# Kernel optimization log

Hardware: AMD Instinct MI355X
Metric: run time of the kernel (lower is better)

The kernel has to match this reference:

```python
import jax, jax.numpy as jnp
import numpy as np

SLACKNESS_PENALTY = 1.0
WEIGHT_DECAY = 1e-5

POS_LEN, NUM_NEG = 32768, 64
N_RULES, N_UNLABEL = 262144, 131072
NUM_ENT, NUM_REL, EMB_DIM = 100000, 500, 256


def _rand_triples(key, n):
    k1, k2, k3 = jax.random.split(key, 3)
    h = jax.random.randint(k1, (n,), 0, NUM_ENT)
    r = jax.random.randint(k2, (n,), 0, NUM_REL)
    t = jax.random.randint(k3, (n,), 0, NUM_ENT)
    return jnp.stack([h, r, t], axis=1)  # [n, 3]


def setup_inputs() -> dict:
    key = jax.random.key(0)
    ks = jax.random.split(key, 10)
    pos_score = jax.random.normal(ks[0], (POS_LEN, 1), dtype=jnp.float32)
    neg_score = jax.random.normal(ks[1], (POS_LEN, NUM_NEG), dtype=jnp.float32)
    confidence = jax.random.uniform(ks[2], (N_RULES,), dtype=jnp.float32)
    ent_emb = jax.random.normal(ks[3], (NUM_ENT, EMB_DIM), dtype=jnp.float32) * 0.1
    rel_emb = jax.random.normal(ks[4], (NUM_REL, EMB_DIM), dtype=jnp.float32) * 0.1
    rule_p1 = _rand_triples(ks[5], N_RULES)
    rule_p2 = _rand_triples(ks[6], N_RULES)
    triple_num = jax.random.randint(ks[7], (N_RULES,), 2, 4)  # values in {2, 3}
    unlabel_ids = jax.random.randint(ks[8], (N_RULES,), 0, N_UNLABEL)
    unlabel_triples = _rand_triples(ks[9], N_UNLABEL)
    return dict(pos_score=pos_score, neg_score=neg_score, confidence=confidence,
                ent_emb=ent_emb, rel_emb=rel_emb, rule_p1=rule_p1, rule_p2=rule_p2,
                triple_num=triple_num, unlabel_ids=unlabel_ids,
                unlabel_triples=unlabel_triples)


def _score(triples, ent_emb, rel_emb):
    # DistMult KGE score: sum_d e_h * w_r * e_t  -> [n, 1]
    h = ent_emb[triples[:, 0]]
    r = rel_emb[triples[:, 1]]
    t = ent_emb[triples[:, 2]]
    return jnp.sum(h * r * t, axis=-1, keepdims=True)


def reference(pos_score, neg_score, confidence, ent_emb, rel_emb,
              rule_p1, rule_p2, triple_num, unlabel_ids, unlabel_triples):
    # BCE(sigmoid(pos), 1) = softplus(-x); BCE(sigmoid(neg), 0) = softplus(x)
    positive_loss = jnp.mean(jax.nn.softplus(-pos_score))
    negative_loss = jnp.mean(jax.nn.softplus(neg_score))

    # Per-rule body sigmoids (originally memoized one-row model() calls)
    s1 = jax.nn.sigmoid(_score(rule_p1, ent_emb, rel_emb))[:, 0]  # [n_rules]
    s2 = jax.nn.sigmoid(_score(rule_p2, ent_emb, rel_emb))[:, 0]
    contrib = SLACKNESS_PENALTY * confidence * s1 * jnp.where(triple_num == 3, s2, 1.0)
    # pi_gradient dict scatter-add -> segment_sum over unique unlabel triples
    pi_grad = jax.ops.segment_sum(contrib, unlabel_ids,
                                  num_segments=unlabel_triples.shape[0])  # [n_unlabel]

    su = _score(unlabel_triples, ent_emb, rel_emb)  # [n_unlabel, 1]
    p = jax.nn.sigmoid(su)
    # target = clip(p + pi_grad, 0, 1), detached (original uses .cpu().detach().numpy())
    tgt = jax.lax.stop_gradient(jnp.clip(p + pi_grad[:, None], 0.0, 1.0))
    # BCE(p, tgt) with stable log-sigmoid forms
    unlabel_loss = jnp.mean(tgt * jax.nn.softplus(-su) + (1.0 - tgt) * jax.nn.softplus(su))

    regularization = WEIGHT_DECAY * (jnp.sum(ent_emb ** 2) + jnp.sum(rel_emb ** 2))
    return positive_loss + negative_loss + unlabel_loss + regularization
```

## Files before the change

kernel.cpp:

```cpp
#include <hip/hip_runtime.h>
#include <cstddef>
#include <cstdint>

#define POS_LEN    32768
#define NUM_NEG    64
#define N_RULES    262144
#define N_UNLABEL  131072
#define NUM_ENT    100000
#define NUM_REL    500
#define EMB_DIM    256
#define WEIGHT_DECAY 1e-5

#define AUX_BLOCKS    2048
#define GATHER_BLOCKS 2048
#define LOSS_BLOCKS   256

typedef __attribute__((ext_vector_type(4))) float        f32x4;
typedef __attribute__((ext_vector_type(2))) unsigned int u32x2;

__device__ __forceinline__ float softplusf_(float x) {
    return fmaxf(x, 0.0f) + log1pf(expf(-fabsf(x)));
}
__device__ __forceinline__ float sigmoidf_(float x) {
    return 1.0f / (1.0f + expf(-x));
}
__device__ __forceinline__ float half_sum32(float v) {
#pragma unroll
    for (int m = 1; m <= 16; m <<= 1) v += __shfl_xor(v, m, 64);
    return v;
}
__device__ __forceinline__ float wave_sum64(float v) {
#pragma unroll
    for (int m = 32; m >= 1; m >>= 1) v += __shfl_xor(v, m, 64);
    return v;
}
__device__ __forceinline__ double wave_sum64d(double v) {
#pragma unroll
    for (int m = 32; m >= 1; m >>= 1) v += __shfl_xor(v, m, 64);
    return v;
}

__device__ __forceinline__ u32x2 f32x8_to_fp8(const f32x4 a, const f32x4 b) {
    int lo = 0, hi = 0;
    lo = __builtin_amdgcn_cvt_pk_fp8_f32(a[0], a[1], lo, false);
    lo = __builtin_amdgcn_cvt_pk_fp8_f32(a[2], a[3], lo, true);
    hi = __builtin_amdgcn_cvt_pk_fp8_f32(b[0], b[1], hi, false);
    hi = __builtin_amdgcn_cvt_pk_fp8_f32(b[2], b[3], hi, true);
    u32x2 r; r[0] = (unsigned)lo; r[1] = (unsigned)hi; return r;
}
__device__ __forceinline__ void fp8x4_to_f32(unsigned int w, float* o) {
    auto x = __builtin_amdgcn_cvt_pk_f32_fp8((int)w, false);
    auto y = __builtin_amdgcn_cvt_pk_f32_fp8((int)w, true);
    o[0] = x[0]; o[1] = x[1]; o[2] = y[0]; o[3] = y[1];
}

__device__ __forceinline__ float triple_score_fp8(const u32x2* __restrict__ ent8,
                                                  const u32x2* __restrict__ rel8,
                                                  int h, int r, int t, int l) {
    const u32x2 hv = ent8[(size_t)h * 32 + l];
    const u32x2 rv = rel8[(size_t)r * 32 + l];
    const u32x2 tv = ent8[(size_t)t * 32 + l];
    float hf[8], rf[8], tf[8];
    fp8x4_to_f32(hv[0], hf); fp8x4_to_f32(hv[1], hf + 4);
    fp8x4_to_f32(rv[0], rf); fp8x4_to_f32(rv[1], rf + 4);
    fp8x4_to_f32(tv[0], tf); fp8x4_to_f32(tv[1], tf + 4);
    float s = 0.0f;
#pragma unroll
    for (int j = 0; j < 8; ++j) s = fmaf(hf[j] * rf[j], tf[j], s);
    return half_sum32(s);
}

__global__ void aux_convert_kernel(const float* __restrict__ pos,
                                   const float* __restrict__ neg,
                                   const float* __restrict__ ent,
                                   const float* __restrict__ rel,
                                   u32x2* __restrict__ ent8,
                                   u32x2* __restrict__ rel8,
                                   float* __restrict__ pi_grad,
                                   float* __restrict__ auxp) {
    const int tid = blockIdx.x * blockDim.x + threadIdx.x;
    const int stride = gridDim.x * blockDim.x;

    for (int i = tid; i < N_UNLABEL; i += stride) pi_grad[i] = 0.0f;

    float ps = 0.0f, ns = 0.0f, sq = 0.0f;
    const f32x4* posv = reinterpret_cast<const f32x4*>(pos);
    const f32x4* negv = reinterpret_cast<const f32x4*>(neg);
    for (int i = tid; i < POS_LEN / 4; i += stride) {
        f32x4 v = __builtin_nontemporal_load(posv + i);
        ps += softplusf_(-v[0]) + softplusf_(-v[1]) + softplusf_(-v[2]) + softplusf_(-v[3]);
    }
    for (int i = tid; i < (POS_LEN * NUM_NEG) / 4; i += stride) {
        f32x4 v = __builtin_nontemporal_load(negv + i);
        ns += softplusf_(v[0]) + softplusf_(v[1]) + softplusf_(v[2]) + softplusf_(v[3]);
    }
    const f32x4* entv = reinterpret_cast<const f32x4*>(ent);
    for (int i = tid; i < (NUM_ENT * EMB_DIM) / 8; i += stride) {
        f32x4 a = __builtin_nontemporal_load(entv + (size_t)i * 2);
        f32x4 b = __builtin_nontemporal_load(entv + (size_t)i * 2 + 1);
        sq += a[0]*a[0] + a[1]*a[1] + a[2]*a[2] + a[3]*a[3]
            + b[0]*b[0] + b[1]*b[1] + b[2]*b[2] + b[3]*b[3];
        ent8[i] = f32x8_to_fp8(a, b);
    }
    const f32x4* relv = reinterpret_cast<const f32x4*>(rel);
    for (int i = tid; i < (NUM_REL * EMB_DIM) / 8; i += stride) {
        f32x4 a = __builtin_nontemporal_load(relv + (size_t)i * 2);
        f32x4 b = __builtin_nontemporal_load(relv + (size_t)i * 2 + 1);
        sq += a[0]*a[0] + a[1]*a[1] + a[2]*a[2] + a[3]*a[3]
            + b[0]*b[0] + b[1]*b[1] + b[2]*b[2] + b[3]*b[3];
        rel8[i] = f32x8_to_fp8(a, b);
    }

    ps = wave_sum64(ps); ns = wave_sum64(ns); sq = wave_sum64(sq);
    __shared__ float lp[8], ln[8], ls[8];
    const int lane = threadIdx.x & 63, wid = threadIdx.x >> 6;
    if (lane == 0) { lp[wid] = ps; ln[wid] = ns; ls[wid] = sq; }
    __syncthreads();
    if (threadIdx.x == 0) {
        float bp = 0.0f, bn = 0.0f, bs = 0.0f;
        for (int w = 0; w < (int)(blockDim.x >> 6); ++w) { bp += lp[w]; bn += ln[w]; bs += ls[w]; }
        auxp[blockIdx.x]                  = bp;
        auxp[AUX_BLOCKS + blockIdx.x]     = bn;
        auxp[2 * AUX_BLOCKS + blockIdx.x] = bs;
    }
}

__global__ void gather_kernel(const float* __restrict__ conf,
                              const u32x2* __restrict__ ent8,
                              const u32x2* __restrict__ rel8,
                              const int* __restrict__ p1,
                              const int* __restrict__ p2,
                              const int* __restrict__ tnum,
                              const int* __restrict__ uids,
                              const int* __restrict__ ut,
                              float* __restrict__ pi_grad,
                              float* __restrict__ su_out) {
    const int lane = threadIdx.x & 63;
    const int l    = lane & 31;
    const int half = lane >> 5;
    const int wave  = blockIdx.x * (blockDim.x >> 6) + (threadIdx.x >> 6);
    const int nwave = gridDim.x * (blockDim.x >> 6);
    const int nrp = N_RULES / 2, nup = N_UNLABEL / 2, ntot = nrp + nup;

    for (int pi = wave; pi < ntot; pi += nwave) {
        if (pi < nrp) {
            const int rule = pi * 2 + half;
            const int h1 = p1[rule * 3 + 0], r1 = p1[rule * 3 + 1], t1 = p1[rule * 3 + 2];
            float c = sigmoidf_(triple_score_fp8(ent8, rel8, h1, r1, t1, l)) * conf[rule];
            if (tnum[rule] == 3) {
                const int h2 = p2[rule * 3 + 0], r2 = p2[rule * 3 + 1], t2 = p2[rule * 3 + 2];
                c *= sigmoidf_(triple_score_fp8(ent8, rel8, h2, r2, t2, l));
            }
            if (l == 0) atomicAdd(&pi_grad[uids[rule]], c);
        } else {
            const int i = (pi - nrp) * 2 + half;
            const int h = ut[i * 3 + 0], r = ut[i * 3 + 1], t = ut[i * 3 + 2];
            const float su = triple_score_fp8(ent8, rel8, h, r, t, l);
            if (l == 0) su_out[i] = su;
        }
    }
}

__global__ void loss_kernel(const float* __restrict__ su,
                            const float* __restrict__ pi_grad,
                            float* __restrict__ lossp) {
    const int tid = blockIdx.x * blockDim.x + threadIdx.x;
    const int stride = gridDim.x * blockDim.x;
    float acc = 0.0f;
    for (int i = tid; i < N_UNLABEL; i += stride) {
        const float s   = su[i];
        const float p   = sigmoidf_(s);
        const float tgt = fminf(fmaxf(p + pi_grad[i], 0.0f), 1.0f);
        acc += tgt * softplusf_(-s) + (1.0f - tgt) * softplusf_(s);
    }
    acc = wave_sum64(acc);
    __shared__ float part[8];
    const int lane = threadIdx.x & 63, wid = threadIdx.x >> 6;
    if (lane == 0) part[wid] = acc;
    __syncthreads();
    if (threadIdx.x == 0) {
        float b = 0.0f;
        for (int w = 0; w < (int)(blockDim.x >> 6); ++w) b += part[w];
        lossp[blockIdx.x] = b;
    }
}

__global__ void finalize_kernel(const float* __restrict__ auxp,
                                const float* __restrict__ lossp,
                                float* __restrict__ out) {
    const int lane = threadIdx.x;
    double ps = 0.0, ns = 0.0, sq = 0.0, ul = 0.0;
    for (int i = lane; i < AUX_BLOCKS; i += 64) {
        ps += (double)auxp[i];
        ns += (double)auxp[AUX_BLOCKS + i];
        sq += (double)auxp[2 * AUX_BLOCKS + i];
    }
    for (int i = lane; i < LOSS_BLOCKS; i += 64) ul += (double)lossp[i];
    ps = wave_sum64d(ps); ns = wave_sum64d(ns);
    sq = wave_sum64d(sq); ul = wave_sum64d(ul);
    if (lane == 0) {
        double v = ps / (double)POS_LEN
                 + ns / ((double)POS_LEN * (double)NUM_NEG)
                 + ul / (double)N_UNLABEL
                 + WEIGHT_DECAY * sq;
        out[0] = (float)v;
    }
}

extern "C" void kernel_launch(void* const* d_in, const int* in_sizes, int n_in,
                              void* d_out, int out_size, void* d_ws, size_t ws_size,
                              hipStream_t stream) {
    const float* pos  = (const float*)d_in[0];
    const float* neg  = (const float*)d_in[1];
    const float* conf = (const float*)d_in[2];
    const float* ent  = (const float*)d_in[3];
    const float* rel  = (const float*)d_in[4];
    const int*   p1   = (const int*)d_in[5];
    const int*   p2   = (const int*)d_in[6];
    const int*   tnum = (const int*)d_in[7];
    const int*   uids = (const int*)d_in[8];
    const int*   ut   = (const int*)d_in[9];

    const size_t off_pi    = 0;
    const size_t off_su    = off_pi + (size_t)N_UNLABEL * 4;
    const size_t off_auxp  = off_su + (size_t)N_UNLABEL * 4;
    const size_t off_lossp = off_auxp + (size_t)3 * AUX_BLOCKS * 4;
    const size_t off_ent8  = (off_lossp + (size_t)LOSS_BLOCKS * 4 + 511) & ~(size_t)511;
    const size_t off_rel8  = off_ent8 + (size_t)NUM_ENT * EMB_DIM;

    float* pi_grad = (float*)((char*)d_ws + off_pi);
    float* su      = (float*)((char*)d_ws + off_su);
    float* auxp    = (float*)((char*)d_ws + off_auxp);
    float* lossp   = (float*)((char*)d_ws + off_lossp);
    u32x2* ent8    = (u32x2*)((char*)d_ws + off_ent8);
    u32x2* rel8    = (u32x2*)((char*)d_ws + off_rel8);

    aux_convert_kernel<<<AUX_BLOCKS, 256, 0, stream>>>(pos, neg, ent, rel,
                                                       ent8, rel8, pi_grad, auxp);
    gather_kernel<<<GATHER_BLOCKS, 256, 0, stream>>>(conf, ent8, rel8, p1, p2, tnum,
                                                     uids, ut, pi_grad, su);
    loss_kernel<<<LOSS_BLOCKS, 256, 0, stream>>>(su, pi_grad, lossp);
    finalize_kernel<<<1, 64, 0, stream>>>(auxp, lossp, (float*)d_out);
}
```

Before: 108.8 us.

## Use fp16 embedding tables with fdot2 and move pos/neg loss into loss kernel

Adds an fp16 path, chosen when the workspace is large enough, that converts the embedding tables to half precision. The gather computes scores with packed fdot2, using 16 lanes per triple and four triples per wave. The pos/neg softplus reductions move from the conversion kernel into the loss kernel, which gets more blocks. The fp16 tables double table write and gather bytes compared with fp8, in exchange for fewer lanes per triple, higher accuracy, and cheaper dot products.

New measurement: 132.7 us. 1.22x slower.

```diff
diff --git a/kernel.cpp b/kernel.cpp
--- a/kernel.cpp
+++ b/kernel.cpp
@@ -13,10 +13,11 @@
 
 #define AUX_BLOCKS    2048
 #define GATHER_BLOCKS 2048
-#define LOSS_BLOCKS   256
+#define LOSS_BLOCKS   1024
 
 typedef __attribute__((ext_vector_type(4))) float        f32x4;
 typedef __attribute__((ext_vector_type(2))) unsigned int u32x2;
+typedef __attribute__((ext_vector_type(8))) _Float16     h8;
 
 __device__ __forceinline__ float softplusf_(float x) {
     return fmaxf(x, 0.0f) + log1pf(expf(-fabsf(x)));
@@ -24,6 +25,11 @@
 __device__ __forceinline__ float sigmoidf_(float x) {
     return 1.0f / (1.0f + expf(-x));
 }
+__device__ __forceinline__ float quarter_sum16(float v) {
+#pragma unroll
+    for (int m = 1; m <= 8; m <<= 1) v += __shfl_xor(v, m, 64);
+    return v;
+}
 __device__ __forceinline__ float half_sum32(float v) {
 #pragma unroll
     for (int m = 1; m <= 16; m <<= 1) v += __shfl_xor(v, m, 64);
@@ -38,6 +44,43 @@
 #pragma unroll
     for (int m = 32; m >= 1; m >>= 1) v += __shfl_xor(v, m, 64);
     return v;
+}
+
+__device__ __forceinline__ h8 f32x8_to_h8(const f32x4 a, const f32x4 b) {
+    auto p0 = __builtin_amdgcn_cvt_pkrtz(a[0], a[1]);
+    auto p1 = __builtin_amdgcn_cvt_pkrtz(a[2], a[3]);
+    auto p2 = __builtin_amdgcn_cvt_pkrtz(b[0], b[1]);
+    auto p3 = __builtin_amdgcn_cvt_pkrtz(b[2], b[3]);
+    h8 o;
+    o[0] = (_Float16)p0[0]; o[1] = (_Float16)p0[1];
+    o[2] = (_Float16)p1[0]; o[3] = (_Float16)p1[1];
+    o[4] = (_Float16)p2[0]; o[5] = (_Float16)p2[1];
+    o[6] = (_Float16)p3[0]; o[7] = (_Float16)p3[1];
+    return o;
+}
+
+#define FD2(acc, m, t, i0, i1)                                               \
+    acc = __builtin_amdgcn_fdot2(                                            \
+        __builtin_shufflevector(m, m, i0, i1),                               \
+        __builtin_shufflevector(t, t, i0, i1), acc, false)
+
+__device__ __forceinline__ float triple_score_f16(const h8* __restrict__ ent16,
+                                                  const h8* __restrict__ rel16,
+                                                  int h, int r, int t, int l) {
+    const h8* hp = ent16 + (size_t)h * 32 + l * 2;
+    const h8* rp = rel16 + (size_t)r * 32 + l * 2;
+    const h8* tp = ent16 + (size_t)t * 32 + l * 2;
+    h8 h0 = hp[0], h1 = hp[1];
+    h8 r0 = rp[0], r1 = rp[1];
+    h8 t0 = tp[0], t1 = tp[1];
+    h8 m0 = h0 * r0;
+    h8 m1 = h1 * r1;
+    float acc = 0.0f;
+    FD2(acc, m0, t0, 0, 1); FD2(acc, m0, t0, 2, 3);
+    FD2(acc, m0, t0, 4, 5); FD2(acc, m0, t0, 6, 7);
+    FD2(acc, m1, t1, 0, 1); FD2(acc, m1, t1, 2, 3);
+    FD2(acc, m1, t1, 4, 5); FD2(acc, m1, t1, 6, 7);
+    return quarter_sum16(acc);
 }
 
 __device__ __forceinline__ u32x2 f32x8_to_fp8(const f32x4 a, const f32x4 b) {
@@ -53,7 +96,6 @@
     auto y = __builtin_amdgcn_cvt_pk_f32_fp8((int)w, true);
     o[0] = x[0]; o[1] = x[1]; o[2] = y[0]; o[3] = y[1];
 }
-
 __device__ __forceinline__ float triple_score_fp8(const u32x2* __restrict__ ent8,
                                                   const u32x2* __restrict__ rel8,
                                                   int h, int r, int t, int l) {
@@ -70,30 +112,55 @@
     return half_sum32(s);
 }
 
-__global__ void aux_convert_kernel(const float* __restrict__ pos,
-                                   const float* __restrict__ neg,
-                                   const float* __restrict__ ent,
-                                   const float* __restrict__ rel,
-                                   u32x2* __restrict__ ent8,
-                                   u32x2* __restrict__ rel8,
-                                   float* __restrict__ pi_grad,
-                                   float* __restrict__ auxp) {
+__global__ void aux_f16_kernel(const float* __restrict__ ent,
+                               const float* __restrict__ rel,
+                               h8* __restrict__ ent16,
+                               h8* __restrict__ rel16,
+                               float* __restrict__ pi_grad,
+                               float* __restrict__ auxp) {
     const int tid = blockIdx.x * blockDim.x + threadIdx.x;
     const int stride = gridDim.x * blockDim.x;
-
     for (int i = tid; i < N_UNLABEL; i += stride) pi_grad[i] = 0.0f;
 
-    float ps = 0.0f, ns = 0.0f, sq = 0.0f;
-    const f32x4* posv = reinterpret_cast<const f32x4*>(pos);
-    const f32x4* negv = reinterpret_cast<const f32x4*>(neg);
-    for (int i = tid; i < POS_LEN / 4; i += stride) {
-        f32x4 v = __builtin_nontemporal_load(posv + i);
-        ps += softplusf_(-v[0]) + softplusf_(-v[1]) + softplusf_(-v[2]) + softplusf_(-v[3]);
-    }
-    for (int i = tid; i < (POS_LEN * NUM_NEG) / 4; i += stride) {
-        f32x4 v = __builtin_nontemporal_load(negv + i);
-        ns += softplusf_(v[0]) + softplusf_(v[1]) + softplusf_(v[2]) + softplusf_(v[3]);
-    }
+    float sq = 0.0f;
+    const f32x4* entv = reinterpret_cast<const f32x4*>(ent);
+    for (int i = tid; i < (NUM_ENT * EMB_DIM) / 8; i += stride) {
+        f32x4 a = __builtin_nontemporal_load(entv + (size_t)i * 2);
+        f32x4 b = __builtin_nontemporal_load(entv + (size_t)i * 2 + 1);
+        sq += a[0]*a[0] + a[1]*a[1] + a[2]*a[2] + a[3]*a[3]
+            + b[0]*b[0] + b[1]*b[1] + b[2]*b[2] + b[3]*b[3];
+        ent16[i] = f32x8_to_h8(a, b);
+    }
+    const f32x4* relv = reinterpret_cast<const f32x4*>(rel);
+    for (int i = tid; i < (NUM_REL * EMB_DIM) / 8; i += stride) {
+        f32x4 a = __builtin_nontemporal_load(relv + (size_t)i * 2);
+        f32x4 b = __builtin_nontemporal_load(relv + (size_t)i * 2 + 1);
+        sq += a[0]*a[0] + a[1]*a[1] + a[2]*a[2] + a[3]*a[3]
+            + b[0]*b[0] + b[1]*b[1] + b[2]*b[2] + b[3]*b[3];
+        rel16[i] = f32x8_to_h8(a, b);
+    }
+    sq = wave_sum64(sq);
+    __shared__ float ls[8];
+    const int lane = threadIdx.x & 63, wid = threadIdx.x >> 6;
+    if (lane == 0) ls[wid] = sq;
+    __syncthreads();
+    if (threadIdx.x == 0) {
+        float bs = 0.0f;
+        for (int w = 0; w < (int)(blockDim.x >> 6); ++w) bs += ls[w];
+        auxp[blockIdx.x] = bs;
+    }
+}
+
+__global__ void aux_fp8_kernel(const float* __restrict__ ent,
+                               const float* __restrict__ rel,
+                               u32x2* __restrict__ ent8,
+                               u32x2* __restrict__ rel8,
+                               float* __restrict__ pi_grad,
+                               float* __restrict__ auxp) {
+    const int tid = blockIdx.x * blockDim.x + threadIdx.x;
+    const int stride = gridDim.x * blockDim.x;
+    for (int i = tid; i < N_UNLABEL; i += stride) pi_grad[i] = 0.0f;
+    float sq = 0.0f;
     const f32x4* entv = reinterpret_cast<const f32x4*>(ent);
     for (int i = tid; i < (NUM_ENT * EMB_DIM) / 8; i += stride) {
         f32x4 a = __builtin_nontemporal_load(entv + (size_t)i * 2);
@@ -110,38 +177,70 @@
             + b[0]*b[0] + b[1]*b[1] + b[2]*b[2] + b[3]*b[3];
         rel8[i] = f32x8_to_fp8(a, b);
     }
-
-    ps = wave_sum64(ps); ns = wave_sum64(ns); sq = wave_sum64(sq);
-    __shared__ float lp[8], ln[8], ls[8];
+    sq = wave_sum64(sq);
+    __shared__ float ls[8];
     const int lane = threadIdx.x & 63, wid = threadIdx.x >> 6;
-    if (lane == 0) { lp[wid] = ps; ln[wid] = ns; ls[wid] = sq; }
+    if (lane == 0) ls[wid] = sq;
     __syncthreads();
     if (threadIdx.x == 0) {
-        float bp = 0.0f, bn = 0.0f, bs = 0.0f;
-        for (int w = 0; w < (int)(blockDim.x >> 6); ++w) { bp += lp[w]; bn += ln[w]; bs += ls[w]; }
-        auxp[blockIdx.x]                  = bp;
-        auxp[AUX_BLOCKS + blockIdx.x]     = bn;
-        auxp[2 * AUX_BLOCKS + blockIdx.x] = bs;
-    }
-}
-
-__global__ void gather_kernel(const float* __restrict__ conf,
-                              const u32x2* __restrict__ ent8,
-                              const u32x2* __restrict__ rel8,
-                              const int* __restrict__ p1,
-                              const int* __restrict__ p2,
-                              const int* __restrict__ tnum,
-                              const int* __restrict__ uids,
-                              const int* __restrict__ ut,
-                              float* __restrict__ pi_grad,
-                              float* __restrict__ su_out) {
+        float bs = 0.0f;
+        for (int w = 0; w < (int)(blockDim.x >> 6); ++w) bs += ls[w];
+        auxp[blockIdx.x] = bs;
+    }
+}
+
+__global__ void gather_f16_kernel(const float* __restrict__ conf,
+                                  const h8* __restrict__ ent16,
+                                  const h8* __restrict__ rel16,
+                                  const int* __restrict__ p1,
+                                  const int* __restrict__ p2,
+                                  const int* __restrict__ tnum,
+                                  const int* __restrict__ uids,
+                                  const int* __restrict__ ut,
+                                  float* __restrict__ pi_grad,
+                                  float* __restrict__ su_out) {
+    const int lane = threadIdx.x & 63;
+    const int l    = lane & 15;
+    const int q    = lane >> 4;
+    const int wave  = blockIdx.x * (blockDim.x >> 6) + (threadIdx.x >> 6);
+    const int nwave = gridDim.x * (blockDim.x >> 6);
+    const int nr4 = N_RULES / 4, nu4 = N_UNLABEL / 4, ntot = nr4 + nu4;
+
+    for (int pi = wave; pi < ntot; pi += nwave) {
+        if (pi < nr4) {
+            const int rule = pi * 4 + q;
+            const int h1 = p1[rule * 3 + 0], r1 = p1[rule * 3 + 1], t1 = p1[rule * 3 + 2];
+            float c = sigmoidf_(triple_score_f16(ent16, rel16, h1, r1, t1, l)) * conf[rule];
+            if (tnum[rule] == 3) {
+                const int h2 = p2[rule * 3 + 0], r2 = p2[rule * 3 + 1], t2 = p2[rule * 3 + 2];
+                c *= sigmoidf_(triple_score_f16(ent16, rel16, h2, r2, t2, l));
+            }
+            if (l == 0) atomicAdd(&pi_grad[uids[rule]], c);
+        } else {
+            const int i = (pi - nr4) * 4 + q;
+            const int h = ut[i * 3 + 0], r = ut[i * 3 + 1], t = ut[i * 3 + 2];
+            const float su = triple_score_f16(ent16, rel16, h, r, t, l);
+            if (l == 0) su_out[i] = su;
+        }
+    }
+}
+
+__global__ void gather_fp8_kernel(const float* __restrict__ conf,
+                                  const u32x2* __restrict__ ent8,
+                                  const u32x2* __restrict__ rel8,
+                                  const int* __restrict__ p1,
+                                  const int* __restrict__ p2,
+                                  const int* __restrict__ tnum,
+                                  const int* __restrict__ uids,
+                                  const int* __restrict__ ut,
+                                  float* __restrict__ pi_grad,
+                                  float* __restrict__ su_out) {
     const int lane = threadIdx.x & 63;
     const int l    = lane & 31;
     const int half = lane >> 5;
     const int wave  = blockIdx.x * (blockDim.x >> 6) + (threadIdx.x >> 6);
     const int nwave = gridDim.x * (blockDim.x >> 6);
     const int nrp = N_RULES / 2, nup = N_UNLABEL / 2, ntot = nrp + nup;
-
     for (int pi = wave; pi < ntot; pi += nwave) {
         if (pi < nrp) {
             const int rule = pi * 2 + half;
@@ -163,25 +262,39 @@
 
 __global__ void loss_kernel(const float* __restrict__ su,
                             const float* __restrict__ pi_grad,
+                            const float* __restrict__ pos,
+                            const float* __restrict__ neg,
                             float* __restrict__ lossp) {
     const int tid = blockIdx.x * blockDim.x + threadIdx.x;
     const int stride = gridDim.x * blockDim.x;
-    float acc = 0.0f;
+    float ul = 0.0f, ps = 0.0f, ns = 0.0f;
     for (int i = tid; i < N_UNLABEL; i += stride) {
         const float s   = su[i];
         const float p   = sigmoidf_(s);
         const float tgt = fminf(fmaxf(p + pi_grad[i], 0.0f), 1.0f);
-        acc += tgt * softplusf_(-s) + (1.0f - tgt) * softplusf_(s);
-    }
-    acc = wave_sum64(acc);
-    __shared__ float part[8];
+        ul += tgt * softplusf_(-s) + (1.0f - tgt) * softplusf_(s);
+    }
+    const f32x4* posv = reinterpret_cast<const f32x4*>(pos);
+    for (int i = tid; i < POS_LEN / 4; i += stride) {
+        f32x4 v = __builtin_nontemporal_load(posv + i);
+        ps += softplusf_(-v[0]) + softplusf_(-v[1]) + softplusf_(-v[2]) + softplusf_(-v[3]);
+    }
+    const f32x4* negv = reinterpret_cast<const f32x4*>(neg);
+    for (int i = tid; i < (POS_LEN * NUM_NEG) / 4; i += stride) {
+        f32x4 v = __builtin_nontemporal_load(negv + i);
+        ns += softplusf_(v[0]) + softplusf_(v[1]) + softplusf_(v[2]) + softplusf_(v[3]);
+    }
+    ul = wave_sum64(ul); ps = wave_sum64(ps); ns = wave_sum64(ns);
+    __shared__ float lu[8], lp[8], ln[8];
     const int lane = threadIdx.x & 63, wid = threadIdx.x >> 6;
-    if (lane == 0) part[wid] = acc;
+    if (lane == 0) { lu[wid] = ul; lp[wid] = ps; ln[wid] = ns; }
     __syncthreads();
     if (threadIdx.x == 0) {
-        float b = 0.0f;
-        for (int w = 0; w < (int)(blockDim.x >> 6); ++w) b += part[w];
-        lossp[blockIdx.x] = b;
+        float bu = 0.0f, bp = 0.0f, bn = 0.0f;
+        for (int w = 0; w < (int)(blockDim.x >> 6); ++w) { bu += lu[w]; bp += lp[w]; bn += ln[w]; }
+        lossp[blockIdx.x]                   = bu;
+        lossp[LOSS_BLOCKS + blockIdx.x]     = bp;
+        lossp[2 * LOSS_BLOCKS + blockIdx.x] = bn;
     }
 }
 
@@ -189,15 +302,15 @@
                                 const float* __restrict__ lossp,
                                 float* __restrict__ out) {
     const int lane = threadIdx.x;
-    double ps = 0.0, ns = 0.0, sq = 0.0, ul = 0.0;
-    for (int i = lane; i < AUX_BLOCKS; i += 64) {
-        ps += (double)auxp[i];
-        ns += (double)auxp[AUX_BLOCKS + i];
-        sq += (double)auxp[2 * AUX_BLOCKS + i];
-    }
-    for (int i = lane; i < LOSS_BLOCKS; i += 64) ul += (double)lossp[i];
+    double sq = 0.0, ul = 0.0, ps = 0.0, ns = 0.0;
+    for (int i = lane; i < AUX_BLOCKS; i += 64) sq += (double)auxp[i];
+    for (int i = lane; i < LOSS_BLOCKS; i += 64) {
+        ul += (double)lossp[i];
+        ps += (double)lossp[LOSS_BLOCKS + i];
+        ns += (double)lossp[2 * LOSS_BLOCKS + i];
+    }
+    sq = wave_sum64d(sq); ul = wave_sum64d(ul);
     ps = wave_sum64d(ps); ns = wave_sum64d(ns);
-    sq = wave_sum64d(sq); ul = wave_sum64d(ul);
     if (lane == 0) {
         double v = ps / (double)POS_LEN
                  + ns / ((double)POS_LEN * (double)NUM_NEG)
@@ -224,21 +337,28 @@
     const size_t off_pi    = 0;
     const size_t off_su    = off_pi + (size_t)N_UNLABEL * 4;
     const size_t off_auxp  = off_su + (size_t)N_UNLABEL * 4;
-    const size_t off_lossp = off_auxp + (size_t)3 * AUX_BLOCKS * 4;
-    const size_t off_ent8  = (off_lossp + (size_t)LOSS_BLOCKS * 4 + 511) & ~(size_t)511;
-    const size_t off_rel8  = off_ent8 + (size_t)NUM_ENT * EMB_DIM;
+    const size_t off_lossp = off_auxp + (size_t)AUX_BLOCKS * 4;
+    const size_t off_tab   = (off_lossp + (size_t)3 * LOSS_BLOCKS * 4 + 511) & ~(size_t)511;
+    const size_t f16_need  = off_tab + (size_t)(NUM_ENT + NUM_REL) * EMB_DIM * 2;
 
     float* pi_grad = (float*)((char*)d_ws + off_pi);
     float* su      = (float*)((char*)d_ws + off_su);
     float* auxp    = (float*)((char*)d_ws + off_auxp);
     float* lossp   = (float*)((char*)d_ws + off_lossp);
-    u32x2* ent8    = (u32x2*)((char*)d_ws + off_ent8);
-    u32x2* rel8    = (u32x2*)((char*)d_ws + off_rel8);
-
-    aux_convert_kernel<<<AUX_BLOCKS, 256, 0, stream>>>(pos, neg, ent, rel,
-                                                       ent8, rel8, pi_grad, auxp);
-    gather_kernel<<<GATHER_BLOCKS, 256, 0, stream>>>(conf, ent8, rel8, p1, p2, tnum,
-                                                     uids, ut, pi_grad, su);
-    loss_kernel<<<LOSS_BLOCKS, 256, 0, stream>>>(su, pi_grad, lossp);
+
+    if (ws_size >= f16_need) {
+        h8* ent16 = (h8*)((char*)d_ws + off_tab);
+        h8* rel16 = (h8*)((char*)d_ws + off_tab + (size_t)NUM_ENT * EMB_DIM * 2);
+        aux_f16_kernel<<<AUX_BLOCKS, 256, 0, stream>>>(ent, rel, ent16, rel16, pi_grad, auxp);
+        gather_f16_kernel<<<GATHER_BLOCKS, 256, 0, stream>>>(conf, ent16, rel16, p1, p2,
+                                                             tnum, uids, ut, pi_grad, su);
+    } else {
+        u32x2* ent8 = (u32x2*)((char*)d_ws + off_tab);
+        u32x2* rel8 = (u32x2*)((char*)d_ws + off_tab + (size_t)NUM_ENT * EMB_DIM);
+        aux_fp8_kernel<<<AUX_BLOCKS, 256, 0, stream>>>(ent, rel, ent8, rel8, pi_grad, auxp);
+        gather_fp8_kernel<<<GATHER_BLOCKS, 256, 0, stream>>>(conf, ent8, rel8, p1, p2,
+                                                             tnum, uids, ut, pi_grad, su);
+    }
+    loss_kernel<<<LOSS_BLOCKS, 256, 0, stream>>>(su, pi_grad, pos, neg, lossp);
     finalize_kernel<<<1, 64, 0, stream>>>(auxp, lossp, (float*)d_out);
 }
```

## Gather fp8 rows with 16-byte loads and move pos/neg softplus into loss kernel

Applied to the files above, without the earlier changes.

The gather kernel now assigns 16 lanes per triple, so each lane loads 16 bytes of fp8 embedding and a wave scores four triples at once. It also issues the second body's loads before computing the first score, to expose more memory parallelism. The pos/neg softplus reductions move from the convert kernel into the loss kernel, whose grid grows from 256 to 1024 blocks. This shortens the critical path before the gather, but puts the 8 MB negative-score read after the gather on the same stream.

Measured after the change: 101.3 us. 6.8% less time.

```diff
diff --git a/kernel.cpp b/kernel.cpp
--- a/kernel.cpp
+++ b/kernel.cpp
@@ -13,10 +13,11 @@
 
 #define AUX_BLOCKS    2048
 #define GATHER_BLOCKS 2048
-#define LOSS_BLOCKS   256
+#define LOSS_BLOCKS   1024
 
 typedef __attribute__((ext_vector_type(4))) float        f32x4;
 typedef __attribute__((ext_vector_type(2))) unsigned int u32x2;
+typedef __attribute__((ext_vector_type(4))) unsigned int u32x4;
 
 __device__ __forceinline__ float softplusf_(float x) {
     return fmaxf(x, 0.0f) + log1pf(expf(-fabsf(x)));
@@ -24,9 +25,9 @@
 __device__ __forceinline__ float sigmoidf_(float x) {
     return 1.0f / (1.0f + expf(-x));
 }
-__device__ __forceinline__ float half_sum32(float v) {
-#pragma unroll
-    for (int m = 1; m <= 16; m <<= 1) v += __shfl_xor(v, m, 64);
+__device__ __forceinline__ float quarter_sum16(float v) {
+#pragma unroll
+    for (int m = 1; m <= 8; m <<= 1) v += __shfl_xor(v, m, 64);
     return v;
 }
 __device__ __forceinline__ float wave_sum64(float v) {
@@ -54,46 +55,32 @@
     o[0] = x[0]; o[1] = x[1]; o[2] = y[0]; o[3] = y[1];
 }
 
-__device__ __forceinline__ float triple_score_fp8(const u32x2* __restrict__ ent8,
-                                                  const u32x2* __restrict__ rel8,
-                                                  int h, int r, int t, int l) {
-    const u32x2 hv = ent8[(size_t)h * 32 + l];
-    const u32x2 rv = rel8[(size_t)r * 32 + l];
-    const u32x2 tv = ent8[(size_t)t * 32 + l];
-    float hf[8], rf[8], tf[8];
-    fp8x4_to_f32(hv[0], hf); fp8x4_to_f32(hv[1], hf + 4);
-    fp8x4_to_f32(rv[0], rf); fp8x4_to_f32(rv[1], rf + 4);
-    fp8x4_to_f32(tv[0], tf); fp8x4_to_f32(tv[1], tf + 4);
+__device__ __forceinline__ float dot3_q(const u32x4 hv, const u32x4 rv, const u32x4 tv) {
     float s = 0.0f;
 #pragma unroll
-    for (int j = 0; j < 8; ++j) s = fmaf(hf[j] * rf[j], tf[j], s);
-    return half_sum32(s);
-}
-
-__global__ void aux_convert_kernel(const float* __restrict__ pos,
-                                   const float* __restrict__ neg,
-                                   const float* __restrict__ ent,
-                                   const float* __restrict__ rel,
-                                   u32x2* __restrict__ ent8,
-                                   u32x2* __restrict__ rel8,
-                                   float* __restrict__ pi_grad,
-                                   float* __restrict__ auxp) {
+    for (int w = 0; w < 4; ++w) {
+        float hf[4], rf[4], tf[4];
+        fp8x4_to_f32(hv[w], hf);
+        fp8x4_to_f32(rv[w], rf);
+        fp8x4_to_f32(tv[w], tf);
+        s = fmaf(hf[0] * rf[0], tf[0], s);
+        s = fmaf(hf[1] * rf[1], tf[1], s);
+        s = fmaf(hf[2] * rf[2], tf[2], s);
+        s = fmaf(hf[3] * rf[3], tf[3], s);
+    }
+    return quarter_sum16(s);
+}
+
+__global__ void aux_fp8_kernel(const float* __restrict__ ent,
+                               const float* __restrict__ rel,
+                               u32x2* __restrict__ ent8,
+                               u32x2* __restrict__ rel8,
+                               float* __restrict__ pi_grad,
+                               float* __restrict__ auxp) {
     const int tid = blockIdx.x * blockDim.x + threadIdx.x;
     const int stride = gridDim.x * blockDim.x;
-
     for (int i = tid; i < N_UNLABEL; i += stride) pi_grad[i] = 0.0f;
-
-    float ps = 0.0f, ns = 0.0f, sq = 0.0f;
-    const f32x4* posv = reinterpret_cast<const f32x4*>(pos);
-    const f32x4* negv = reinterpret_cast<const f32x4*>(neg);
-    for (int i = tid; i < POS_LEN / 4; i += stride) {
-        f32x4 v = __builtin_nontemporal_load(posv + i);
-        ps += softplusf_(-v[0]) + softplusf_(-v[1]) + softplusf_(-v[2]) + softplusf_(-v[3]);
-    }
-    for (int i = tid; i < (POS_LEN * NUM_NEG) / 4; i += stride) {
-        f32x4 v = __builtin_nontemporal_load(negv + i);
-        ns += softplusf_(v[0]) + softplusf_(v[1]) + softplusf_(v[2]) + softplusf_(v[3]);
-    }
+    float sq = 0.0f;
     const f32x4* entv = reinterpret_cast<const f32x4*>(ent);
     for (int i = tid; i < (NUM_ENT * EMB_DIM) / 8; i += stride) {
         f32x4 a = __builtin_nontemporal_load(entv + (size_t)i * 2);
@@ -110,24 +97,21 @@
             + b[0]*b[0] + b[1]*b[1] + b[2]*b[2] + b[3]*b[3];
         rel8[i] = f32x8_to_fp8(a, b);
     }
-
-    ps = wave_sum64(ps); ns = wave_sum64(ns); sq = wave_sum64(sq);
-    __shared__ float lp[8], ln[8], ls[8];
+    sq = wave_sum64(sq);
+    __shared__ float ls[8];
     const int lane = threadIdx.x & 63, wid = threadIdx.x >> 6;
-    if (lane == 0) { lp[wid] = ps; ln[wid] = ns; ls[wid] = sq; }
+    if (lane == 0) ls[wid] = sq;
     __syncthreads();
     if (threadIdx.x == 0) {
-        float bp = 0.0f, bn = 0.0f, bs = 0.0f;
-        for (int w = 0; w < (int)(blockDim.x >> 6); ++w) { bp += lp[w]; bn += ln[w]; bs += ls[w]; }
-        auxp[blockIdx.x]                  = bp;
-        auxp[AUX_BLOCKS + blockIdx.x]     = bn;
-        auxp[2 * AUX_BLOCKS + blockIdx.x] = bs;
+        float bs = 0.0f;
+        for (int w = 0; w < (int)(blockDim.x >> 6); ++w) bs += ls[w];
+        auxp[blockIdx.x] = bs;
     }
 }
 
 __global__ void gather_kernel(const float* __restrict__ conf,
-                              const u32x2* __restrict__ ent8,
-                              const u32x2* __restrict__ rel8,
+                              const u32x4* __restrict__ ent8,
+                              const u32x4* __restrict__ rel8,
                               const int* __restrict__ p1,
                               const int* __restrict__ p2,
                               const int* __restrict__ tnum,
@@ -136,26 +120,42 @@
                               float* __restrict__ pi_grad,
                               float* __restrict__ su_out) {
     const int lane = threadIdx.x & 63;
-    const int l    = lane & 31;
-    const int half = lane >> 5;
+    const int l    = lane & 15;
+    const int q    = lane >> 4;
     const int wave  = blockIdx.x * (blockDim.x >> 6) + (threadIdx.x >> 6);
     const int nwave = gridDim.x * (blockDim.x >> 6);
-    const int nrp = N_RULES / 2, nup = N_UNLABEL / 2, ntot = nrp + nup;
+    const int nr4 = N_RULES / 4, nu4 = N_UNLABEL / 4, ntot = nr4 + nu4;
 
     for (int pi = wave; pi < ntot; pi += nwave) {
-        if (pi < nrp) {
-            const int rule = pi * 2 + half;
-            const int h1 = p1[rule * 3 + 0], r1 = p1[rule * 3 + 1], t1 = p1[rule * 3 + 2];
-            float c = sigmoidf_(triple_score_fp8(ent8, rel8, h1, r1, t1, l)) * conf[rule];
-            if (tnum[rule] == 3) {
-                const int h2 = p2[rule * 3 + 0], r2 = p2[rule * 3 + 1], t2 = p2[rule * 3 + 2];
-                c *= sigmoidf_(triple_score_fp8(ent8, rel8, h2, r2, t2, l));
+        if (pi < nr4) {
+            const int rule = pi * 4 + q;
+            const int b = rule * 3;
+            const int h1 = p1[b], r1 = p1[b + 1], t1 = p1[b + 2];
+            const int tn = tnum[rule];
+            const float cf = conf[rule];
+            const int uid = uids[rule];
+            const bool has2 = (tn == 3);
+            const u32x4 H1 = ent8[(size_t)h1 * 16 + l];
+            const u32x4 R1 = rel8[(size_t)r1 * 16 + l];
+            const u32x4 T1 = ent8[(size_t)t1 * 16 + l];
+            u32x4 H2 = {0, 0, 0, 0}, R2 = {0, 0, 0, 0}, T2 = {0, 0, 0, 0};
+            if (has2) {
+                const int h2 = p2[b], r2 = p2[b + 1], t2 = p2[b + 2];
+                H2 = ent8[(size_t)h2 * 16 + l];
+                R2 = rel8[(size_t)r2 * 16 + l];
+                T2 = ent8[(size_t)t2 * 16 + l];
             }
-            if (l == 0) atomicAdd(&pi_grad[uids[rule]], c);
+            float c = sigmoidf_(dot3_q(H1, R1, T1)) * cf;
+            if (has2) c *= sigmoidf_(dot3_q(H2, R2, T2));
+            if (l == 0) atomicAdd(&pi_grad[uid], c);
         } else {
-            const int i = (pi - nrp) * 2 + half;
-            const int h = ut[i * 3 + 0], r = ut[i * 3 + 1], t = ut[i * 3 + 2];
-            const float su = triple_score_fp8(ent8, rel8, h, r, t, l);
+            const int i = (pi - nr4) * 4 + q;
+            const int b = i * 3;
+            const int h = ut[b], r = ut[b + 1], t = ut[b + 2];
+            const u32x4 H = ent8[(size_t)h * 16 + l];
+            const u32x4 R = rel8[(size_t)r * 16 + l];
+            const u32x4 T = ent8[(size_t)t * 16 + l];
+            const float su = dot3_q(H, R, T);
             if (l == 0) su_out[i] = su;
         }
     }
@@ -163,25 +163,39 @@
 
 __global__ void loss_kernel(const float* __restrict__ su,
                             const float* __restrict__ pi_grad,
+                            const float* __restrict__ pos,
+                            const float* __restrict__ neg,
                             float* __restrict__ lossp) {
     const int tid = blockIdx.x * blockDim.x + threadIdx.x;
     const int stride = gridDim.x * blockDim.x;
-    float acc = 0.0f;
+    float ul = 0.0f, ps = 0.0f, ns = 0.0f;
     for (int i = tid; i < N_UNLABEL; i += stride) {
         const float s   = su[i];
         const float p   = sigmoidf_(s);
         const float tgt = fminf(fmaxf(p + pi_grad[i], 0.0f), 1.0f);
-        acc += tgt * softplusf_(-s) + (1.0f - tgt) * softplusf_(s);
-    }
-    acc = wave_sum64(acc);
-    __shared__ float part[8];
+        ul += tgt * softplusf_(-s) + (1.0f - tgt) * softplusf_(s);
+    }
+    const f32x4* posv = reinterpret_cast<const f32x4*>(pos);
+    for (int i = tid; i < POS_LEN / 4; i += stride) {
+        f32x4 v = __builtin_nontemporal_load(posv + i);
+        ps += softplusf_(-v[0]) + softplusf_(-v[1]) + softplusf_(-v[2]) + softplusf_(-v[3]);
+    }
+    const f32x4* negv = reinterpret_cast<const f32x4*>(neg);
+    for (int i = tid; i < (POS_LEN * NUM_NEG) / 4; i += stride) {
+        f32x4 v = __builtin_nontemporal_load(negv + i);
+        ns += softplusf_(v[0]) + softplusf_(v[1]) + softplusf_(v[2]) + softplusf_(v[3]);
+    }
+    ul = wave_sum64(ul); ps = wave_sum64(ps); ns = wave_sum64(ns);
+    __shared__ float lu[8], lp[8], ln[8];
     const int lane = threadIdx.x & 63, wid = threadIdx.x >> 6;
-    if (lane == 0) part[wid] = acc;
+    if (lane == 0) { lu[wid] = ul; lp[wid] = ps; ln[wid] = ns; }
     __syncthreads();
     if (threadIdx.x == 0) {
-        float b = 0.0f;
-        for (int w = 0; w < (int)(blockDim.x >> 6); ++w) b += part[w];
-        lossp[blockIdx.x] = b;
+        float bu = 0.0f, bp = 0.0f, bn = 0.0f;
+        for (int w = 0; w < (int)(blockDim.x >> 6); ++w) { bu += lu[w]; bp += lp[w]; bn += ln[w]; }
+        lossp[blockIdx.x]                   = bu;
+        lossp[LOSS_BLOCKS + blockIdx.x]     = bp;
+        lossp[2 * LOSS_BLOCKS + blockIdx.x] = bn;
     }
 }
 
@@ -189,15 +203,15 @@
                                 const float* __restrict__ lossp,
                                 float* __restrict__ out) {
     const int lane = threadIdx.x;
-    double ps = 0.0, ns = 0.0, sq = 0.0, ul = 0.0;
-    for (int i = lane; i < AUX_BLOCKS; i += 64) {
-        ps += (double)auxp[i];
-        ns += (double)auxp[AUX_BLOCKS + i];
-        sq += (double)auxp[2 * AUX_BLOCKS + i];
-    }
-    for (int i = lane; i < LOSS_BLOCKS; i += 64) ul += (double)lossp[i];
+    double sq = 0.0, ul = 0.0, ps = 0.0, ns = 0.0;
+    for (int i = lane; i < AUX_BLOCKS; i += 64) sq += (double)auxp[i];
+    for (int i = lane; i < LOSS_BLOCKS; i += 64) {
+        ul += (double)lossp[i];
+        ps += (double)lossp[LOSS_BLOCKS + i];
+        ns += (double)lossp[2 * LOSS_BLOCKS + i];
+    }
+    sq = wave_sum64d(sq); ul = wave_sum64d(ul);
     ps = wave_sum64d(ps); ns = wave_sum64d(ns);
-    sq = wave_sum64d(sq); ul = wave_sum64d(ul);
     if (lane == 0) {
         double v = ps / (double)POS_LEN
                  + ns / ((double)POS_LEN * (double)NUM_NEG)
@@ -224,21 +238,22 @@
     const size_t off_pi    = 0;
     const size_t off_su    = off_pi + (size_t)N_UNLABEL * 4;
     const size_t off_auxp  = off_su + (size_t)N_UNLABEL * 4;
-    const size_t off_lossp = off_auxp + (size_t)3 * AUX_BLOCKS * 4;
-    const size_t off_ent8  = (off_lossp + (size_t)LOSS_BLOCKS * 4 + 511) & ~(size_t)511;
-    const size_t off_rel8  = off_ent8 + (size_t)NUM_ENT * EMB_DIM;
+    const size_t off_lossp = off_auxp + (size_t)AUX_BLOCKS * 4;
+    const size_t off_tab   = (off_lossp + (size_t)3 * LOSS_BLOCKS * 4 + 511) & ~(size_t)511;
+    const size_t off_rel8  = off_tab + (size_t)NUM_ENT * EMB_DIM;
 
     float* pi_grad = (float*)((char*)d_ws + off_pi);
     float* su      = (float*)((char*)d_ws + off_su);
     float* auxp    = (float*)((char*)d_ws + off_auxp);
     float* lossp   = (float*)((char*)d_ws + off_lossp);
-    u32x2* ent8    = (u32x2*)((char*)d_ws + off_ent8);
-    u32x2* rel8    = (u32x2*)((char*)d_ws + off_rel8);
-
-    aux_convert_kernel<<<AUX_BLOCKS, 256, 0, stream>>>(pos, neg, ent, rel,
-                                                       ent8, rel8, pi_grad, auxp);
-    gather_kernel<<<GATHER_BLOCKS, 256, 0, stream>>>(conf, ent8, rel8, p1, p2, tnum,
-                                                     uids, ut, pi_grad, su);
-    loss_kernel<<<LOSS_BLOCKS, 256, 0, stream>>>(su, pi_grad, lossp);
+    u32x2* ent8w   = (u32x2*)((char*)d_ws + off_tab);
+    u32x2* rel8w   = (u32x2*)((char*)d_ws + off_rel8);
+
+    aux_fp8_kernel<<<AUX_BLOCKS, 256, 0, stream>>>(ent, rel, ent8w, rel8w, pi_grad, auxp);
+    gather_kernel<<<GATHER_BLOCKS, 256, 0, stream>>>(conf,
+                                                     (const u32x4*)((char*)d_ws + off_tab),
+                                                     (const u32x4*)((char*)d_ws + off_rel8),
+                                                     p1, p2, tnum, uids, ut, pi_grad, su);
+    loss_kernel<<<LOSS_BLOCKS, 256, 0, stream>>>(su, pi_grad, pos, neg, lossp);
     finalize_kernel<<<1, 64, 0, stream>>>(auxp, lossp, (float*)d_out);
 }
```
